# Kernel tuning notes

Measured on AMD Instinct MI355X. Metric: run time of the kernel, lower is better.

The kernel has to match this reference:

```python
import jax, jax.numpy as jnp
import numpy as np

N = 50000      # nodes
E = 800000     # edges
D = 128        # input_dim
H = 128        # hidden_dim
OUT = 86       # output_dim (DDI classes)
P = 100000     # drug pairs
BN_EPS = 1e-5


def setup_inputs() -> dict:
    key = jax.random.key(0)
    ks = jax.random.split(key, 16)
    s = 0.05
    return {
        "x": jax.random.normal(ks[0], (N, D), jnp.float32),
        "edge_index": jax.random.randint(ks[1], (2, E), 0, N),
        "drug_pairs": jax.random.randint(ks[2], (P, 2), 0, N),
        # GCN layer 1 (input_dim -> hidden_dim) + BatchNorm params
        "W1": jax.random.normal(ks[3], (D, H), jnp.float32) * s,
        "b1": jnp.zeros((H,), jnp.float32),
        "gamma1": jnp.ones((H,), jnp.float32),
        "beta1": jnp.zeros((H,), jnp.float32),
        # GCN layer 2 (hidden -> hidden) + BatchNorm params
        "W2": jax.random.normal(ks[4], (H, H), jnp.float32) * s,
        "b2": jnp.zeros((H,), jnp.float32),
        "gamma2": jnp.ones((H,), jnp.float32),
        "beta2": jnp.zeros((H,), jnp.float32),
        # edge classifier MLP: Linear(2H,H) -> ReLU -> Linear(H,H//2) -> ReLU -> Linear(H//2,OUT)
        "Wc1": jax.random.normal(ks[5], (2 * H, H), jnp.float32) * s,
        "bc1": jnp.zeros((H,), jnp.float32),
        "Wc2": jax.random.normal(ks[6], (H, H // 2), jnp.float32) * s,
        "bc2": jnp.zeros((H // 2,), jnp.float32),
        "Wc3": jax.random.normal(ks[7], (H // 2, OUT), jnp.float32) * s,
        "bc3": jnp.zeros((OUT,), jnp.float32),
    }


def gcn_conv(h, W, b, src, dst, n):
    """PyG GCNConv: D^-1/2 (A + I) D^-1/2 (h @ W) + b, with self-loops added."""
    h = h @ W  # [N, H]
    ones = jnp.ones(src.shape[0], h.dtype)
    deg = jax.ops.segment_sum(ones, dst, num_segments=n) + 1.0  # in-degree + self loop
    dinv = jax.lax.rsqrt(deg)  # [N]
    coef = dinv[src] * dinv[dst]  # [E] edge normalization
    agg = jax.ops.segment_sum(h[src] * coef[:, None], dst, num_segments=n)
    agg = agg + h * (dinv * dinv)[:, None]  # self-loop contribution: deg_i^-1 * h_i
    return agg + b


def batch_norm(h, gamma, beta):
    # training-mode BatchNorm1d over node dim (biased variance)
    mean = jnp.mean(h, axis=0)
    var = jnp.mean((h - mean) ** 2, axis=0)
    return gamma * (h - mean) * jax.lax.rsqrt(var + BN_EPS) + beta


def reference(x, edge_index, drug_pairs, W1, b1, gamma1, beta1,
              W2, b2, gamma2, beta2, Wc1, bc1, Wc2, bc2, Wc3, bc3):
    src, dst = edge_index[0], edge_index[1]
    n = x.shape[0]
    # layer 1
    h = jax.nn.relu(batch_norm(gcn_conv(x, W1, b1, src, dst, n), gamma1, beta1))
    # layer 2
    h = jax.nn.relu(batch_norm(gcn_conv(h, W2, b2, src, dst, n), gamma2, beta2))
    # node-pair gather + concat -> edge classifier MLP (dropout = identity in eval)
    combined = jnp.concatenate([h[drug_pairs[:, 0]], h[drug_pairs[:, 1]]], axis=1)  # [P, 2H]
    z = jax.nn.relu(combined @ Wc1 + bc1)
    z = jax.nn.relu(z @ Wc2 + bc2)
    return z @ Wc3 + bc3  # [P, OUT]
```

## Files before the change

### kernel.cpp

```cpp
#include <hip/hip_runtime.h>
#include <cstdint>

#define N_NODES 50000
#define N_EDGES 800000
#define NPAIRS  100000

typedef unsigned short u16;
typedef unsigned int u32;
typedef _Float16 f16;
typedef short short8v __attribute__((ext_vector_type(8)));
typedef _Float16 h8 __attribute__((ext_vector_type(8)));
typedef _Float16 h4 __attribute__((ext_vector_type(4)));
typedef float f32x4 __attribute__((ext_vector_type(4)));

static __device__ __forceinline__ u16 f2bf(float f) {
  unsigned int u = __float_as_uint(f);
  u += 0x7FFF + ((u >> 16) & 1);
  return (u16)(u >> 16);
}

static __device__ __forceinline__ float bits2f(u32 hi) {
  union { u16 b; f16 h; } x;
  x.b = (u16)hi;
  return (float)x.h;
}


__global__ __launch_bounds__(256) void pre_k(const int* __restrict__ ei, int* __restrict__ deg, int* __restrict__ rank,
                                             const float* __restrict__ W1, const float* __restrict__ W2,
                                             const float* __restrict__ Wc1, const float* __restrict__ Wc2,
                                             const float* __restrict__ Wc3,
                                             f16* __restrict__ W1F, f16* __restrict__ W2F,
                                             u16* __restrict__ Wc1F, u16* __restrict__ Wc2F, u16* __restrict__ Wc3F) {
  int b = blockIdx.x;
  if (b < N_EDGES / 256) {
    int e = b * 256 + threadIdx.x;
    rank[e] = atomicAdd(&deg[ei[N_EDGES + e]], 1);
    return;
  }
  int slot = (b - N_EDGES / 256) * 256 + threadIdx.x;
  int lane = slot & 63, j = lane & 15, kg = lane >> 4;
  if (slot < 2048) {
    int ks = (slot >> 6) & 3, nt = slot >> 8;
    int k0 = ks * 32 + kg * 8, c = nt * 16 + j;
#pragma unroll
    for (int e = 0; e < 8; e++) W1F[(size_t)slot * 8 + e] = (f16)W1[(k0 + e) * 128 + c];
  } else if (slot < 4096) {
    int s2 = slot - 2048;
    int ks = (s2 >> 6) & 3, nt = s2 >> 8;
    int k0 = ks * 32 + kg * 8, c = nt * 16 + j;
#pragma unroll
    for (int e = 0; e < 8; e++) W2F[(size_t)s2 * 8 + e] = (f16)W2[(k0 + e) * 128 + c];
  } else if (slot < 8192) {
    int s3 = slot - 4096;
    int ks = (s3 >> 6) & 7, nt = s3 >> 9;
    int k0 = ks * 32 + kg * 8, c = nt * 16 + j;
#pragma unroll
    for (int e = 0; e < 8; e++) Wc1F[(size_t)s3 * 8 + e] = f2bf(Wc1[(k0 + e) * 128 + c]);
  } else if (slot < 9216) {
    int s4 = slot - 8192;
    int ks = (s4 >> 6) & 3, nt = s4 >> 8;
    int k0 = ks * 32 + kg * 8, c = nt * 16 + j;
#pragma unroll
    for (int e = 0; e < 8; e++) Wc2F[(size_t)s4 * 8 + e] = f2bf(Wc2[(k0 + e) * 64 + c]);
  } else if (slot < 10240) {
    int s5 = slot - 9216;
    int ks = (s5 >> 6) & 1, nt = s5 >> 7;
    int k0 = ks * 32 + kg * 8, c = nt * 16 + j;
#pragma unroll
    for (int e = 0; e < 8; e++)
      Wc3F[(size_t)s5 * 8 + e] = f2bf((c < 86) ? Wc3[(k0 + e) * 86 + c] : 0.f);
  }
}

__global__ __launch_bounds__(1024) void scan_k(const int* __restrict__ deg, int* __restrict__ offs,
                                               float* __restrict__ dinv, int n) {
  __shared__ int wsum[16];
  __shared__ int wpre[16];
  __shared__ int run_s;
  int tid = threadIdx.x, lane = tid & 63, wid = tid >> 6;
  if (tid == 0) run_s = 0;
  __syncthreads();
  for (int base = 0; base < n; base += 4096) {
    int i4 = base + tid * 4;
    int4 v = make_int4(0, 0, 0, 0);
    if (i4 + 3 < n) v = *(const int4*)&deg[i4];
    else {
      if (i4 < n) v.x = deg[i4];
      if (i4 + 1 < n) v.y = deg[i4 + 1];
      if (i4 + 2 < n) v.z = deg[i4 + 2];
      if (i4 + 3 < n) v.w = deg[i4 + 3];
    }
    int tsum = v.x + v.y + v.z + v.w;
    int s = tsum;
#pragma unroll
    for (int d = 1; d < 64; d <<= 1) {
      int t = __shfl_up(s, d);
      if (lane >= d) s += t;
    }
    if (lane == 63) wsum[wid] = s;
    __syncthreads();
    if (tid == 0) {
      int acc = run_s;
#pragma unroll
      for (int w = 0; w < 16; w++) { wpre[w] = acc; acc += wsum[w]; }
      run_s = acc;
    }
    __syncthreads();
    int pre = wpre[wid] + (s - tsum);
    int4 o;
    o.x = pre; o.y = pre + v.x; o.z = o.y + v.y; o.w = o.z + v.z;
    float4 dv;
    dv.x = rsqrtf((float)v.x + 1.0f);
    dv.y = rsqrtf((float)v.y + 1.0f);
    dv.z = rsqrtf((float)v.z + 1.0f);
    dv.w = rsqrtf((float)v.w + 1.0f);
    if (i4 + 3 < n) {
      *(int4*)&offs[i4] = o;
      *(float4*)&dinv[i4] = dv;
    } else {
      if (i4 < n)     { offs[i4] = o.x;     dinv[i4] = dv.x; }
      if (i4 + 1 < n) { offs[i4 + 1] = o.y; dinv[i4 + 1] = dv.y; }
      if (i4 + 2 < n) { offs[i4 + 2] = o.z; dinv[i4 + 2] = dv.z; }
      if (i4 + 3 < n) { offs[i4 + 3] = o.w; dinv[i4 + 3] = dv.w; }
    }
    __syncthreads();
  }
  if (tid == 0) offs[n] = run_s;
}

__global__ __launch_bounds__(256) void fill_k(const int* __restrict__ ei, const int* __restrict__ offs,
                                              const int* __restrict__ rank, const float* __restrict__ dinv,
                                              u32* __restrict__ csrp, int E) {
  int e = blockIdx.x * 256 + threadIdx.x;
  if (e < E) {
    int s = ei[e], d = ei[E + e];
    int idx = offs[d] + rank[e];
    f16 hv = (f16)dinv[s];
    u32 pack = (u32)(u16)s | ((u32)(*(u16*)&hv) << 16);
    csrp[idx] = pack;
  }
}


template<int MODE>
__global__ __launch_bounds__(256) void gemm_mfma_k(const void* __restrict__ Ain,
                                                   const float* __restrict__ sums,
                                                   const float* __restrict__ gamma,
                                                   const float* __restrict__ beta,
                                                   const f16* __restrict__ WF,
                                                   f16* __restrict__ outh, int n) {
  __shared__ f16 As[64 * 136];
  __shared__ float scsh[256];
  int tid = threadIdx.x;
  if (MODE == 1) {
    if (tid < 128) {
      const float inv_n = 1.0f / (float)N_NODES;
      float mean = sums[tid] * inv_n;
      float var = sums[128 + tid] * inv_n - mean * mean;
      float sc = gamma[tid] * rsqrtf(var + 1e-5f);
      scsh[tid] = sc;
      scsh[128 + tid] = beta[tid] - mean * sc;
    }
    __syncthreads();
  }
  int row0 = blockIdx.x * 64;
#pragma unroll
  for (int it = 0; it < 8; it++) {
    int idx = it * 256 + tid;
    int r = idx >> 5, c4 = (idx & 31) * 4;
    int gr = row0 + r; if (gr >= n) gr = n - 1;
    float4 v;
    if (MODE == 0) {
      v = *(const float4*)&((const float*)Ain)[(size_t)gr * 128 + c4];
    } else {
      h4 hv4 = *(const h4*)&((const f16*)Ain)[(size_t)gr * 128 + c4];
      v.x = (float)hv4[0]; v.y = (float)hv4[1]; v.z = (float)hv4[2]; v.w = (float)hv4[3];
      v.x = fmaxf(v.x * scsh[c4 + 0] + scsh[128 + c4 + 0], 0.f);
      v.y = fmaxf(v.y * scsh[c4 + 1] + scsh[128 + c4 + 1], 0.f);
      v.z = fmaxf(v.z * scsh[c4 + 2] + scsh[128 + c4 + 2], 0.f);
      v.w = fmaxf(v.w * scsh[c4 + 3] + scsh[128 + c4 + 3], 0.f);
    }
    h4 hv; hv[0] = (f16)v.x; hv[1] = (f16)v.y; hv[2] = (f16)v.z; hv[3] = (f16)v.w;
    *(h4*)&As[r * 136 + c4] = hv;
  }
  __syncthreads();
  int w = tid >> 6, lane = tid & 63, li = lane & 15, kg = lane >> 4;
  f32x4 acc[4][2];
#pragma unroll
  for (int mt = 0; mt < 4; mt++)
#pragma unroll
    for (int ntl = 0; ntl < 2; ntl++)
#pragma unroll
      for (int q = 0; q < 4; q++) acc[mt][ntl][q] = 0.f;
#pragma unroll
  for (int ks = 0; ks < 4; ks++) {
    h8 a[4];
#pragma unroll
    for (int mt = 0; mt < 4; mt++)
      a[mt] = *(const h8*)&As[(mt * 16 + li) * 136 + kg * 8 + ks * 32];
#pragma unroll
    for (int ntl = 0; ntl < 2; ntl++) {
      int nt = 2 * w + ntl;
      h8 b = *(const h8*)&WF[((size_t)(nt * 4 + ks) * 64 + lane) * 8];
#pragma unroll
      for (int mt = 0; mt < 4; mt++)
        acc[mt][ntl] = __builtin_amdgcn_mfma_f32_16x16x32_f16(a[mt], b, acc[mt][ntl], 0, 0, 0);
    }
  }
  __syncthreads();
#pragma unroll
  for (int mt = 0; mt < 4; mt++)
#pragma unroll
    for (int ntl = 0; ntl < 2; ntl++)
#pragma unroll
      for (int r = 0; r < 4; r++)
        As[(mt * 16 + kg * 4 + r) * 136 + (2 * w + ntl) * 16 + li] = (f16)acc[mt][ntl][r];
  __syncthreads();
#pragma unroll
  for (int it = 0; it < 4; it++) {
    int idx = it * 256 + tid;
    int r = idx >> 4, c8 = (idx & 15) * 8;
    int gr = row0 + r;
    if (gr < n) *(h8*)&outh[(size_t)gr * 128 + c8] = *(const h8*)&As[r * 136 + c8];
  }
}


__global__ __launch_bounds__(256) void agg_h_k(const f16* __restrict__ th, const float* __restrict__ dinv,
                                               const int* __restrict__ offs, const u32* __restrict__ csrp,
                                               const float* __restrict__ bias, f16* __restrict__ outh,
                                               float* __restrict__ sums, int n) {
  int tid = threadIdx.x;
  int lane = tid & 63, w = tid >> 6;
  const u32* hu = (const u32*)th;
  u32* ou = (u32*)outh;
  float bx = bias[lane * 2], by = bias[lane * 2 + 1];
  float s1x = 0.f, s1y = 0.f, q1x = 0.f, q1y = 0.f;
  union CV { u32 u; f16 h[2]; };
  for (int node = blockIdx.x * 4 + w; node < n; node += gridDim.x * 4) {
    float di = dinv[node];
    int e0 = offs[node], e1 = offs[node + 1];
    float a0x = 0.f, a0y = 0.f, a1x = 0.f, a1y = 0.f;
    float a2x = 0.f, a2y = 0.f, a3x = 0.f, a3y = 0.f;
    int e = e0;
    for (; e + 4 <= e1; e += 4) {
      u32 p0 = csrp[e], p1 = csrp[e + 1], p2 = csrp[e + 2], p3 = csrp[e + 3];
      float c0 = bits2f(p0 >> 16), c1 = bits2f(p1 >> 16);
      float c2 = bits2f(p2 >> 16), c3 = bits2f(p3 >> 16);
      CV v0, v1, v2, v3;
      v0.u = hu[(size_t)(p0 & 0xFFFF) * 64 + lane];
      v1.u = hu[(size_t)(p1 & 0xFFFF) * 64 + lane];
      v2.u = hu[(size_t)(p2 & 0xFFFF) * 64 + lane];
      v3.u = hu[(size_t)(p3 & 0xFFFF) * 64 + lane];
      a0x += c0 * (float)v0.h[0]; a0y += c0 * (float)v0.h[1];
      a1x += c1 * (float)v1.h[0]; a1y += c1 * (float)v1.h[1];
      a2x += c2 * (float)v2.h[0]; a2y += c2 * (float)v2.h[1];
      a3x += c3 * (float)v3.h[0]; a3y += c3 * (float)v3.h[1];
    }
    for (; e < e1; e++) {
      u32 p0 = csrp[e];
      float c0 = bits2f(p0 >> 16);
      CV v0; v0.u = hu[(size_t)(p0 & 0xFFFF) * 64 + lane];
      a0x += c0 * (float)v0.h[0]; a0y += c0 * (float)v0.h[1];
    }
    float sx = (a0x + a1x) + (a2x + a3x);
    float sy = (a0y + a1y) + (a2y + a3y);
    CV vs; vs.u = hu[(size_t)node * 64 + lane];
    float sc = di * di;
    float rx = di * sx + sc * (float)vs.h[0] + bx;
    float ry = di * sy + sc * (float)vs.h[1] + by;
    CV o; o.h[0] = (f16)rx; o.h[1] = (f16)ry;
    ou[(size_t)node * 64 + lane] = o.u;
    s1x += rx; q1x += rx * rx;
    s1y += ry; q1y += ry * ry;
  }
  __shared__ float rsum[4][128];
  __shared__ float rsq[4][128];
  rsum[w][lane * 2] = s1x; rsum[w][lane * 2 + 1] = s1y;
  rsq[w][lane * 2] = q1x;  rsq[w][lane * 2 + 1] = q1y;
  __syncthreads();
  if (tid < 128) {
    float a = (rsum[0][tid] + rsum[1][tid]) + (rsum[2][tid] + rsum[3][tid]);
    float b = (rsq[0][tid] + rsq[1][tid]) + (rsq[2][tid] + rsq[3][tid]);
    atomicAdd(&sums[tid], a);
    atomicAdd(&sums[128 + tid], b);
  }
}


__global__ __launch_bounds__(256) void bn_apply_bf16_k(const f16* __restrict__ h, const float* __restrict__ sums,
                                                       const float* __restrict__ gamma, const float* __restrict__ beta,
                                                       u16* __restrict__ hb) {
  __shared__ float scsh[256];
  int tid = threadIdx.x;
  if (tid < 128) {
    const float inv_n = 1.0f / (float)N_NODES;
    float mean = sums[tid] * inv_n;
    float var = sums[128 + tid] * inv_n - mean * mean;
    float sc = gamma[tid] * rsqrtf(var + 1e-5f);
    scsh[tid] = sc;
    scsh[128 + tid] = beta[tid] - mean * sc;
  }
  __syncthreads();
  int idx = blockIdx.x * 256 + tid;
  int c0 = (idx & 31) * 4;
  h4 v4 = *(const h4*)&h[(size_t)idx * 4];
  ushort4 o;
  o.x = f2bf(fmaxf((float)v4[0] * scsh[c0 + 0] + scsh[128 + c0 + 0], 0.f));
  o.y = f2bf(fmaxf((float)v4[1] * scsh[c0 + 1] + scsh[128 + c0 + 1], 0.f));
  o.z = f2bf(fmaxf((float)v4[2] * scsh[c0 + 2] + scsh[128 + c0 + 2], 0.f));
  o.w = f2bf(fmaxf((float)v4[3] * scsh[c0 + 3] + scsh[128 + c0 + 3], 0.f));
  *(ushort4*)&hb[(size_t)idx * 4] = o;
}


#define SM_Z1 33792
#define SM_TOT (33792 + 17408)

__global__ __launch_bounds__(256) void classifier_k(const u16* __restrict__ hbf, const int* __restrict__ pairs,
    const u16* __restrict__ Wc1F, const float* __restrict__ bc1,
    const u16* __restrict__ Wc2F, const float* __restrict__ bc2,
    const u16* __restrict__ Wc3F, const float* __restrict__ bc3,
    float* __restrict__ out) {
  __shared__ __align__(16) char smem[SM_TOT];
  __shared__ int nodes[128];
  int tid = threadIdx.x;
  int p0 = blockIdx.x * 64;
  if (tid < 128) {
    int gi = p0 * 2 + tid;
    nodes[tid] = (gi < NPAIRS * 2) ? pairs[gi] : 0;
  }
  __syncthreads();
  int w = tid >> 6, lane = tid & 63;
  int li = lane & 15, kg = lane >> 4;

  {
    unsigned int* cmb = (unsigned int*)smem;
    for (int s = w * 32; s < w * 32 + 32; s++) {
      int nd = nodes[s];
      unsigned int v = ((const unsigned int*)hbf)[(size_t)nd * 64 + lane];
      cmb[(s >> 1) * 132 + (s & 1) * 64 + lane] = v;
    }
  }
  __syncthreads();

  {
    f32x4 acc[4][2];
#pragma unroll
    for (int ntl = 0; ntl < 2; ntl++) {
      float b = bc1[(2 * w + ntl) * 16 + li];
#pragma unroll
      for (int mt = 0; mt < 4; mt++)
#pragma unroll
        for (int q = 0; q < 4; q++) acc[mt][ntl][q] = b;
    }
    for (int ks = 0; ks < 8; ks++) {
      short8v a[4];
#pragma unroll
      for (int mt = 0; mt < 4; mt++)
        a[mt] = *(const short8v*)(smem + (mt * 16 + li) * 528 + kg * 16 + ks * 64);
#pragma unroll
      for (int ntl = 0; ntl < 2; ntl++) {
        int nt = 2 * w + ntl;
        short8v b = *(const short8v*)(Wc1F + ((size_t)(nt * 8 + ks) * 64 + lane) * 8);
#pragma unroll
        for (int mt = 0; mt < 4; mt++)
          acc[mt][ntl] = __builtin_amdgcn_mfma_f32_16x16x32_bf16(a[mt], b, acc[mt][ntl], 0, 0, 0);
      }
    }
#pragma unroll
    for (int mt = 0; mt < 4; mt++)
#pragma unroll
      for (int ntl = 0; ntl < 2; ntl++)
#pragma unroll
        for (int r = 0; r < 4; r++) {
          int row = mt * 16 + kg * 4 + r;
          int col = (2 * w + ntl) * 16 + li;
          *(u16*)(smem + SM_Z1 + row * 272 + col * 2) = f2bf(fmaxf(acc[mt][ntl][r], 0.f));
        }
  }
  __syncthreads();

  {
    f32x4 acc[4];
    float b = bc2[w * 16 + li];
#pragma unroll
    for (int mt = 0; mt < 4; mt++)
#pragma unroll
      for (int q = 0; q < 4; q++) acc[mt][q] = b;
    for (int ks = 0; ks < 4; ks++) {
      short8v a[4];
#pragma unroll
      for (int mt = 0; mt < 4; mt++)
        a[mt] = *(const short8v*)(smem + SM_Z1 + (mt * 16 + li) * 272 + kg * 16 + ks * 64);
      short8v bf = *(const short8v*)(Wc2F + ((size_t)(w * 4 + ks) * 64 + lane) * 8);
#pragma unroll
      for (int mt = 0; mt < 4; mt++)
        acc[mt] = __builtin_amdgcn_mfma_f32_16x16x32_bf16(a[mt], bf, acc[mt], 0, 0, 0);
    }
#pragma unroll
    for (int mt = 0; mt < 4; mt++)
#pragma unroll
      for (int r = 0; r < 4; r++) {
        int row = mt * 16 + kg * 4 + r;
        int col = w * 16 + li;
        *(u16*)(smem + row * 144 + col * 2) = f2bf(fmaxf(acc[mt][r], 0.f));
      }
  }
  __syncthreads();

  {
    f32x4 acc[4][2];
#pragma unroll
    for (int ntl = 0; ntl < 2; ntl++) {
      int col = (2 * w + ntl) * 16 + li;
      float b = (col < 86) ? bc3[col] : 0.f;
#pragma unroll
      for (int mt = 0; mt < 4; mt++)
#pragma unroll
        for (int q = 0; q < 4; q++) acc[mt][ntl][q] = b;
    }
    for (int ks = 0; ks < 2; ks++) {
      short8v a[4];
#pragma unroll
      for (int mt = 0; mt < 4; mt++)
        a[mt] = *(const short8v*)(smem + (mt * 16 + li) * 144 + kg * 16 + ks * 64);
#pragma unroll
      for (int ntl = 0; ntl < 2; ntl++) {
        int nt = 2 * w + ntl;
        short8v bf = *(const short8v*)(Wc3F + ((size_t)(nt * 2 + ks) * 64 + lane) * 8);
#pragma unroll
        for (int mt = 0; mt < 4; mt++)
          acc[mt][ntl] = __builtin_amdgcn_mfma_f32_16x16x32_bf16(a[mt], bf, acc[mt][ntl], 0, 0, 0);
      }
    }
#pragma unroll
    for (int mt = 0; mt < 4; mt++)
#pragma unroll
      for (int ntl = 0; ntl < 2; ntl++) {
        int col = (2 * w + ntl) * 16 + li;
        if (col < 86) {
#pragma unroll
          for (int r = 0; r < 4; r++) {
            int row = p0 + mt * 16 + kg * 4 + r;
            if (row < NPAIRS) out[(size_t)row * 86 + col] = acc[mt][ntl][r];
          }
        }
      }
  }
}


extern "C" void kernel_launch(void* const* d_in, const int* in_sizes, int n_in,
                              void* d_out, int out_size, void* d_ws, size_t ws_size,
                              hipStream_t stream) {
  (void)in_sizes; (void)n_in; (void)out_size; (void)ws_size;
  const float* x   = (const float*)d_in[0];
  const int*   ei  = (const int*)d_in[1];
  const int* pairs = (const int*)d_in[2];
  const float* W1  = (const float*)d_in[3];
  const float* b1  = (const float*)d_in[4];
  const float* g1  = (const float*)d_in[5];
  const float* be1 = (const float*)d_in[6];
  const float* W2  = (const float*)d_in[7];
  const float* b2  = (const float*)d_in[8];
  const float* g2  = (const float*)d_in[9];
  const float* be2 = (const float*)d_in[10];
  const float* Wc1 = (const float*)d_in[11];
  const float* bc1 = (const float*)d_in[12];
  const float* Wc2 = (const float*)d_in[13];
  const float* bc2 = (const float*)d_in[14];
  const float* Wc3 = (const float*)d_in[15];
  const float* bc3 = (const float*)d_in[16];
  float* out = (float*)d_out;

  size_t off = 0;
  auto alloc = [&](size_t bytes) -> char* {
    char* p = (char*)d_ws + off;
    off += (bytes + 255) & ~(size_t)255;
    return p;
  };
  int* deg      = (int*)alloc(N_NODES * 4);
  float* sums1  = (float*)alloc(256 * 4);
  float* sums2  = (float*)alloc(256 * 4);
  size_t zero_span = off;
  int* offs     = (int*)alloc((N_NODES + 1) * 4);
  int* rank     = (int*)alloc(N_EDGES * 4);
  u32* csrp     = (u32*)alloc(N_EDGES * 4);
  float* dinv   = (float*)alloc(N_NODES * 4);
  f16* W1F      = (f16*)alloc(2048 * 8 * 2);
  f16* W2F      = (f16*)alloc(2048 * 8 * 2);
  u16* Wc1F     = (u16*)alloc(4096 * 8 * 2);
  u16* Wc2F     = (u16*)alloc(1024 * 8 * 2);
  u16* Wc3F     = (u16*)alloc(1024 * 8 * 2);
  f16* th       = (f16*)alloc((size_t)N_NODES * 128 * 2);
  f16* hA       = (f16*)alloc((size_t)N_NODES * 128 * 2);
  u16* hbf      = (u16*)th;

  hipMemsetAsync(d_ws, 0, zero_span, stream);
  pre_k<<<N_EDGES / 256 + 40, 256, 0, stream>>>(ei, deg, rank, W1, W2, Wc1, Wc2, Wc3,
                                                W1F, W2F, Wc1F, Wc2F, Wc3F);
  scan_k<<<1, 1024, 0, stream>>>(deg, offs, dinv, N_NODES);
  fill_k<<<N_EDGES / 256, 256, 0, stream>>>(ei, offs, rank, dinv, csrp, N_EDGES);

  gemm_mfma_k<0><<<(N_NODES + 63) / 64, 256, 0, stream>>>(x, nullptr, nullptr, nullptr, W1F, th, N_NODES);
  agg_h_k<<<2048, 256, 0, stream>>>(th, dinv, offs, csrp, b1, hA, sums1, N_NODES);

  gemm_mfma_k<1><<<(N_NODES + 63) / 64, 256, 0, stream>>>(hA, sums1, g1, be1, W2F, th, N_NODES);
  agg_h_k<<<2048, 256, 0, stream>>>(th, dinv, offs, csrp, b2, hA, sums2, N_NODES);

  bn_apply_bf16_k<<<(N_NODES * 128) / 1024, 256, 0, stream>>>(hA, sums2, g2, be2, hbf);

  classifier_k<<<(NPAIRS + 63) / 64, 256, 0, stream>>>(hbf, pairs, Wc1F, bc1, Wc2F, bc2, Wc3F, bc3, out);
}
```

Measured before the change: 390.2 us.

## Split aggregation into per-node wavefronts with 8-byte loads and separate BN stats kernel

The aggregation kernel now gives each wavefront exactly one node. The two half-waves process alternating edges with 8-byte feature loads and are combined with a shuffle, and the grid-stride loop is gone. The batch-norm sum and sum-of-squares accumulation moves out of the aggregation kernel into a new stats kernel that re-reads the aggregated output. This is meant to raise memory-level parallelism in the gather and cut per-node loop overhead, at the cost of an extra full read of the hidden activations and an extra launch per layer.

```diff
diff --git a/kernel.cpp b/kernel.cpp
--- a/kernel.cpp
+++ b/kernel.cpp
@@ -7,6 +7,7 @@
 
 typedef unsigned short u16;
 typedef unsigned int u32;
+typedef unsigned long long u64;
 typedef _Float16 f16;
 typedef short short8v __attribute__((ext_vector_type(8)));
 typedef _Float16 h8 __attribute__((ext_vector_type(8)));
@@ -229,56 +230,86 @@
 
 __global__ __launch_bounds__(256) void agg_h_k(const f16* __restrict__ th, const float* __restrict__ dinv,
                                                const int* __restrict__ offs, const u32* __restrict__ csrp,
-                                               const float* __restrict__ bias, f16* __restrict__ outh,
-                                               float* __restrict__ sums, int n) {
+                                               const float* __restrict__ bias, f16* __restrict__ outh, int n) {
   int tid = threadIdx.x;
-  int lane = tid & 63, w = tid >> 6;
-  const u32* hu = (const u32*)th;
-  u32* ou = (u32*)outh;
-  float bx = bias[lane * 2], by = bias[lane * 2 + 1];
-  float s1x = 0.f, s1y = 0.f, q1x = 0.f, q1y = 0.f;
+  int w = tid >> 6, lane = tid & 63;
+  int half = lane >> 5, sl = lane & 31;
+  int node = blockIdx.x * 4 + w;
+  if (node >= n) return;
+  const u64* hu8 = (const u64*)th;
+  float di = dinv[node];
+  int e0 = offs[node], e1 = offs[node + 1];
+  union C8 { u64 u; f16 h[4]; };
+  float a0[4] = {0.f, 0.f, 0.f, 0.f};
+  float a1[4] = {0.f, 0.f, 0.f, 0.f};
+  float a2[4] = {0.f, 0.f, 0.f, 0.f};
+  float a3[4] = {0.f, 0.f, 0.f, 0.f};
+  int e = e0;
+  for (; e + 8 <= e1; e += 8) {
+    u32 p0 = csrp[e + half];
+    u32 p1 = csrp[e + 2 + half];
+    u32 p2 = csrp[e + 4 + half];
+    u32 p3 = csrp[e + 6 + half];
+    C8 v0, v1, v2, v3;
+    v0.u = hu8[(size_t)(p0 & 0xFFFF) * 32 + sl];
+    v1.u = hu8[(size_t)(p1 & 0xFFFF) * 32 + sl];
+    v2.u = hu8[(size_t)(p2 & 0xFFFF) * 32 + sl];
+    v3.u = hu8[(size_t)(p3 & 0xFFFF) * 32 + sl];
+    float c0 = bits2f(p0 >> 16), c1 = bits2f(p1 >> 16);
+    float c2 = bits2f(p2 >> 16), c3 = bits2f(p3 >> 16);
+#pragma unroll
+    for (int j = 0; j < 4; j++) {
+      a0[j] += c0 * (float)v0.h[j];
+      a1[j] += c1 * (float)v1.h[j];
+      a2[j] += c2 * (float)v2.h[j];
+      a3[j] += c3 * (float)v3.h[j];
+    }
+  }
+  for (; e < e1; e += 2) {
+    int ee = e + half;
+    bool valid = ee < e1;
+    u32 p0 = csrp[valid ? ee : e];
+    float c0 = valid ? bits2f(p0 >> 16) : 0.f;
+    C8 v0; v0.u = hu8[(size_t)(p0 & 0xFFFF) * 32 + sl];
+#pragma unroll
+    for (int j = 0; j < 4; j++) a0[j] += c0 * (float)v0.h[j];
+  }
+  float s[4];
+#pragma unroll
+  for (int j = 0; j < 4; j++) {
+    s[j] = (a0[j] + a1[j]) + (a2[j] + a3[j]);
+    s[j] += __shfl_xor(s[j], 32);
+  }
+  if (half == 0) {
+    C8 vs; vs.u = hu8[(size_t)node * 32 + sl];
+    float4 b4 = *(const float4*)&bias[sl * 4];
+    float sc = di * di;
+    C8 o;
+    o.h[0] = (f16)(di * s[0] + sc * (float)vs.h[0] + b4.x);
+    o.h[1] = (f16)(di * s[1] + sc * (float)vs.h[1] + b4.y);
+    o.h[2] = (f16)(di * s[2] + sc * (float)vs.h[2] + b4.z);
+    o.h[3] = (f16)(di * s[3] + sc * (float)vs.h[3] + b4.w);
+    ((u64*)outh)[(size_t)node * 32 + sl] = o.u;
+  }
+}
+
+
+__global__ __launch_bounds__(256) void bn_stats_h_k(const f16* __restrict__ h, float* __restrict__ sums, int n) {
+  int tid = threadIdx.x;
+  int c = tid & 63, rg = tid >> 6;
+  const u32* hu = (const u32*)h;
   union CV { u32 u; f16 h[2]; };
-  for (int node = blockIdx.x * 4 + w; node < n; node += gridDim.x * 4) {
-    float di = dinv[node];
-    int e0 = offs[node], e1 = offs[node + 1];
-    float a0x = 0.f, a0y = 0.f, a1x = 0.f, a1y = 0.f;
-    float a2x = 0.f, a2y = 0.f, a3x = 0.f, a3y = 0.f;
-    int e = e0;
-    for (; e + 4 <= e1; e += 4) {
-      u32 p0 = csrp[e], p1 = csrp[e + 1], p2 = csrp[e + 2], p3 = csrp[e + 3];
-      float c0 = bits2f(p0 >> 16), c1 = bits2f(p1 >> 16);
-      float c2 = bits2f(p2 >> 16), c3 = bits2f(p3 >> 16);
-      CV v0, v1, v2, v3;
-      v0.u = hu[(size_t)(p0 & 0xFFFF) * 64 + lane];
-      v1.u = hu[(size_t)(p1 & 0xFFFF) * 64 + lane];
-      v2.u = hu[(size_t)(p2 & 0xFFFF) * 64 + lane];
-      v3.u = hu[(size_t)(p3 & 0xFFFF) * 64 + lane];
-      a0x += c0 * (float)v0.h[0]; a0y += c0 * (float)v0.h[1];
-      a1x += c1 * (float)v1.h[0]; a1y += c1 * (float)v1.h[1];
-      a2x += c2 * (float)v2.h[0]; a2y += c2 * (float)v2.h[1];
-      a3x += c3 * (float)v3.h[0]; a3y += c3 * (float)v3.h[1];
-    }
-    for (; e < e1; e++) {
-      u32 p0 = csrp[e];
-      float c0 = bits2f(p0 >> 16);
-      CV v0; v0.u = hu[(size_t)(p0 & 0xFFFF) * 64 + lane];
-      a0x += c0 * (float)v0.h[0]; a0y += c0 * (float)v0.h[1];
-    }
-    float sx = (a0x + a1x) + (a2x + a3x);
-    float sy = (a0y + a1y) + (a2y + a3y);
-    CV vs; vs.u = hu[(size_t)node * 64 + lane];
-    float sc = di * di;
-    float rx = di * sx + sc * (float)vs.h[0] + bx;
-    float ry = di * sy + sc * (float)vs.h[1] + by;
-    CV o; o.h[0] = (f16)rx; o.h[1] = (f16)ry;
-    ou[(size_t)node * 64 + lane] = o.u;
-    s1x += rx; q1x += rx * rx;
-    s1y += ry; q1y += ry * ry;
+  float sx = 0.f, sy = 0.f, qx = 0.f, qy = 0.f;
+  for (int r = blockIdx.x * 4 + rg; r < n; r += gridDim.x * 4) {
+    CV v; v.u = hu[(size_t)r * 64 + c];
+    float x = (float)v.h[0], y = (float)v.h[1];
+    sx += x; qx += x * x;
+    sy += y; qy += y * y;
   }
   __shared__ float rsum[4][128];
   __shared__ float rsq[4][128];
-  rsum[w][lane * 2] = s1x; rsum[w][lane * 2 + 1] = s1y;
-  rsq[w][lane * 2] = q1x;  rsq[w][lane * 2 + 1] = q1y;
+  rsum[rg][c * 2] = sx; rsum[rg][c * 2 + 1] = sy;
+  rsq[rg][c * 2] = qx;  rsq[rg][c * 2 + 1] = qy;
   __syncthreads();
   if (tid < 128) {
     float a = (rsum[0][tid] + rsum[1][tid]) + (rsum[2][tid] + rsum[3][tid]);
@@ -505,10 +536,12 @@
   fill_k<<<N_EDGES / 256, 256, 0, stream>>>(ei, offs, rank, dinv, csrp, N_EDGES);
 
   gemm_mfma_k<0><<<(N_NODES + 63) / 64, 256, 0, stream>>>(x, nullptr, nullptr, nullptr, W1F, th, N_NODES);
-  agg_h_k<<<2048, 256, 0, stream>>>(th, dinv, offs, csrp, b1, hA, sums1, N_NODES);
+  agg_h_k<<<(N_NODES + 3) / 4, 256, 0, stream>>>(th, dinv, offs, csrp, b1, hA, N_NODES);
+  bn_stats_h_k<<<256, 256, 0, stream>>>(hA, sums1, N_NODES);
 
   gemm_mfma_k<1><<<(N_NODES + 63) / 64, 256, 0, stream>>>(hA, sums1, g1, be1, W2F, th, N_NODES);
-  agg_h_k<<<2048, 256, 0, stream>>>(th, dinv, offs, csrp, b2, hA, sums2, N_NODES);
+  agg_h_k<<<(N_NODES + 3) / 4, 256, 0, stream>>>(th, dinv, offs, csrp, b2, hA, N_NODES);
+  bn_stats_h_k<<<256, 256, 0, stream>>>(hA, sums2, N_NODES);
 
   bn_apply_bf16_k<<<(N_NODES * 128) / 1024, 256, 0, stream>>>(hA, sums2, g2, be2, hbf);
 
```

New measurement: 335.8 us. 1.16x faster.
